# Performance work log

Hardware: AMD Instinct MI355X
Metric: run time of the kernel (lower is better)

The kernel has to match this reference:

```python
import jax, jax.numpy as jnp
import numpy as np

K = 64                      # sort-pool k
B_GRAPHS, N_PER = 256, 512  # graphs, nodes per graph
DIM_F, E_PER = 128, 8192    # node feature dim, edges per graph
EMB = 32


def setup_inputs() -> dict:
    key = jax.random.key(0)
    ks = jax.random.split(key, 12)
    N = B_GRAPHS * N_PER
    off = (jnp.arange(B_GRAPHS) * N_PER)[:, None]
    x = jax.random.normal(ks[0], (N, DIM_F), jnp.float32)
    edge_src = (jax.random.randint(ks[1], (B_GRAPHS, E_PER), 0, N_PER) + off).reshape(-1)
    edge_dst = (jax.random.randint(ks[2], (B_GRAPHS, E_PER), 0, N_PER) + off).reshape(-1)

    def lin(k, o, i):
        return (jax.random.normal(k, (o, i), jnp.float32) / np.float32(np.sqrt(i)))

    return {
        "x": x,
        "W0": lin(ks[3], EMB, DIM_F), "b0": jnp.zeros((EMB,), jnp.float32),
        "W1": lin(ks[4], EMB, EMB),   "b1": jnp.zeros((EMB,), jnp.float32),
        "W2": lin(ks[5], EMB, EMB),   "b2": jnp.zeros((EMB,), jnp.float32),
        "W3": lin(ks[6], 1, EMB),     "b3": jnp.zeros((1,), jnp.float32),
        "conv1_w": jax.random.normal(ks[7], (16, 1, 97), jnp.float32) / np.float32(np.sqrt(97.0)),
        "conv1_b": jnp.zeros((16,), jnp.float32),
        "conv2_w": jax.random.normal(ks[8], (32, 16, 5), jnp.float32) / np.float32(np.sqrt(80.0)),
        "conv2_b": jnp.zeros((32,), jnp.float32),
        "d1_w": lin(ks[9], 128, 896),  "d1_b": jnp.zeros((128,), jnp.float32),
        "d2_w": lin(ks[10], 10, 128),  "d2_b": jnp.zeros((10,), jnp.float32),
        "edge_src": edge_src, "edge_dst": edge_dst,
        "num_graphs": B_GRAPHS,
    }


def _dgcnn_conv(h_in, W, b, src, dst):
    # h = lin(x); message = (1/deg_src)[dst] * h[src]; scatter-add at dst
    N = h_in.shape[0]
    h = h_in @ W.T + b
    deg = jax.ops.segment_sum(jnp.ones_like(src, dtype=h.dtype), src, num_segments=N)
    norm = 1.0 / deg                       # self-loops guarantee deg >= 1
    msg = h[src] * norm[dst][:, None]      # [E+N, C]
    return jax.ops.segment_sum(msg, dst, num_segments=N)


def _forward(x, W0, b0, W1, b1, W2, b2, W3, b3,
             conv1_w, conv1_b, conv2_w, conv2_b,
             d1_w, d1_b, d2_w, d2_b, src, dst, num_graphs):
    N = x.shape[0]
    self_idx = jnp.arange(N)
    src = jnp.concatenate([src, self_idx])   # add_self_loops
    dst = jnp.concatenate([dst, self_idx])
    hs = []
    h = x
    for (W, b) in ((W0, b0), (W1, b1), (W2, b2), (W3, b3)):
        h = jnp.tanh(_dgcnn_conv(h, W, b, src, dst))
        hs.append(h)
    feat = jnp.concatenate(hs, axis=1)       # [N, 97]
    D = feat.shape[1]
    B = num_graphs
    n = N // B
    g = feat.reshape(B, n, D)
    # global_sort_pool: sort nodes per graph by last channel, descending, take top-k
    order = jnp.argsort(-g[:, :, -1], axis=1)[:, :K]
    topk = jnp.take_along_axis(g, order[:, :, None], axis=1)   # [B, K, D]
    # Conv1d(1,16,kernel=D,stride=D) over [B,1,K*D] == per-node linear on D
    c1 = jax.nn.relu(jnp.einsum('bkd,od->bok', topk, conv1_w[:, 0, :])
                     + conv1_b[None, :, None])                  # [B,16,K]
    p = c1.reshape(B, 16, K // 2, 2).max(axis=-1)               # MaxPool1d(2,2)
    c2 = jax.lax.conv_general_dilated(p, conv2_w, (1,), 'VALID',
                                      dimension_numbers=('NCH', 'OIH', 'NCH'))
    c2 = jax.nn.relu(c2 + conv2_b[None, :, None])               # [B,32,28]
    flat = c2.reshape(B, -1)                                    # [B,896]
    hid = jax.nn.relu(flat @ d1_w.T + d1_b)                     # dropout = identity (eval)
    return hid @ d2_w.T + d2_b                                  # [B,10]


def reference(x, W0, b0, W1, b1, W2, b2, W3, b3,
              conv1_w, conv1_b, conv2_w, conv2_b,
              d1_w, d1_b, d2_w, d2_b, edge_src, edge_dst, num_graphs):
    return _forward(x, W0, b0, W1, b1, W2, b2, W3, b3,
                    conv1_w, conv1_b, conv2_w, conv2_b,
                    d1_w, d1_b, d2_w, d2_b, edge_src, edge_dst, num_graphs)
```

## Files before the change

kernel.cpp:

```cpp
#include <hip/hip_runtime.h>

#define NG   256
#define NP   512
#define EPG  8192
#define FDIM 128
#define STA  33
#define STB  36

#define OFF_BUFA  0
#define OFF_BUFB  67584
#define OFF_CSR   141312
#define OFF_OFFS  157696
#define OFF_WT    158728
#define OFF_DCNT  158760
#define OFF_NRM   160808
#define SMEM_SZ   162856

#define OFF_KEYA OFF_CSR
#define OFF_IDXA (OFF_CSR + 2048)
#define OFF_KEYB (OFF_CSR + 4096)
#define OFF_IDXB (OFF_CSR + 6144)
#define FO_FEAT 0
#define FO_C1   6208
#define FO_P    7232
#define FO_C2   7744
#define FO_HID  8640

__global__ __launch_bounds__(1024, 4) void dgcnn_fused(
    const float* __restrict__ x,
    const float* __restrict__ W0, const float* __restrict__ b0,
    const float* __restrict__ W1, const float* __restrict__ b1,
    const float* __restrict__ W2, const float* __restrict__ b2,
    const float* __restrict__ W3, const float* __restrict__ b3,
    const float* __restrict__ c1w, const float* __restrict__ c1b,
    const float* __restrict__ c2w, const float* __restrict__ c2b,
    const float* __restrict__ d1w, const float* __restrict__ d1b,
    const float* __restrict__ d2w, const float* __restrict__ d2b,
    const int* __restrict__ esrc, const int* __restrict__ edst,
    float* __restrict__ hs1, float* __restrict__ hs2,
    float* __restrict__ out)
{
  extern __shared__ char smem[];
  float*          stageF = (float*)(smem + OFF_BUFA);
  float*          bufA  = (float*)(smem + OFF_BUFA);
  float*          bufB  = (float*)(smem + OFF_BUFB);
  unsigned short* csr   = (unsigned short*)(smem + OFF_CSR);
  unsigned short* offs  = (unsigned short*)(smem + OFF_OFFS);
  unsigned int*   wt    = (unsigned int*)(smem + OFF_WT);
  unsigned int*   dcnt  = (unsigned int*)(smem + OFF_DCNT);
  float*          nrm   = (float*)(smem + OFF_NRM);
  float*          lin3S = (float*)(smem + OFF_DCNT);
  float*          keyA  = (float*)(smem + OFF_KEYA);
  unsigned int*   idxA  = (unsigned int*)(smem + OFF_IDXA);
  float*          keyB  = (float*)(smem + OFF_KEYB);
  unsigned int*   idxB  = (unsigned int*)(smem + OFF_IDXB);

  const int g    = blockIdx.x;
  const int tid  = threadIdx.x;
  const int lane = tid & 63;
  const int wv   = __builtin_amdgcn_readfirstlane(tid >> 6);
  const int half = __builtin_amdgcn_readfirstlane(tid >> 9);
  const int v    = tid & 511;
  const int nb   = g * NP;
  const size_t gb = (size_t)g * (NP * 32);

  const int ldRow0 = tid >> 3;
  const int ldGrp  = tid & 7;
  const int ldSwz  = (ldGrp ^ (ldRow0 & 7)) * 16;
  const float* xp0 = x + (size_t)nb * FDIM + ldGrp * 4 + (size_t)(ldRow0      ) * FDIM;
  const float* xp1 = x + (size_t)nb * FDIM + ldGrp * 4 + (size_t)(ldRow0 + 128) * FDIM;
  const float* xp2 = x + (size_t)nb * FDIM + ldGrp * 4 + (size_t)(ldRow0 + 256) * FDIM;
  const float* xp3 = x + (size_t)nb * FDIM + ldGrp * 4 + (size_t)(ldRow0 + 384) * FDIM;
  char* sp0 = smem + OFF_BUFA + (ldRow0      ) * 128 + ldSwz;
  char* sp1 = smem + OFF_BUFA + (ldRow0 + 128) * 128 + ldSwz;
  char* sp2 = smem + OFF_BUFA + (ldRow0 + 256) * 128 + ldSwz;
  char* sp3 = smem + OFF_BUFA + (ldRow0 + 384) * 128 + ldSwz;
#define LOADC(kc, r0, r1, r2, r3)                         \
  { r0 = *(const float4*)(xp0 + (kc) * 32);               \
    r1 = *(const float4*)(xp1 + (kc) * 32);               \
    r2 = *(const float4*)(xp2 + (kc) * 32);               \
    r3 = *(const float4*)(xp3 + (kc) * 32); }
#define STOREC(r0, r1, r2, r3)                            \
  { *(float4*)sp0 = r0; *(float4*)sp1 = r1;               \
    *(float4*)sp2 = r2; *(float4*)sp3 = r3; }

  float4 xA0, xA1, xA2, xA3, xB0, xB1, xB2, xB3;
  LOADC(0, xA0, xA1, xA2, xA3);

  if (tid < 512) dcnt[tid] = 0u;
  __syncthreads();

  int es[8], ed[8];
  {
    const int eb = g * EPG;
    const int4* s4 = (const int4*)(esrc + eb);
    const int4* d4 = (const int4*)(edst + eb);
    const int4 sa = s4[tid], sb = s4[tid + 1024];
    const int4 da = d4[tid], db = d4[tid + 1024];
    es[0]=sa.x-nb; es[1]=sa.y-nb; es[2]=sa.z-nb; es[3]=sa.w-nb;
    es[4]=sb.x-nb; es[5]=sb.y-nb; es[6]=sb.z-nb; es[7]=sb.w-nb;
    ed[0]=da.x-nb; ed[1]=da.y-nb; ed[2]=da.z-nb; ed[3]=da.w-nb;
    ed[4]=db.x-nb; ed[5]=db.y-nb; ed[6]=db.z-nb; ed[7]=db.w-nb;
#pragma unroll
    for (int i = 0; i < 8; i++) {
      atomicAdd(&dcnt[es[i]], 1u);
      atomicAdd(&dcnt[ed[i]], 65536u);
    }
  }
  __syncthreads();

  unsigned c_scan = 0;
  if (tid < 512) {
    const unsigned cw = dcnt[tid];
    nrm[tid] = 1.0f / (float)((cw & 0xFFFFu) + 1u);
    dcnt[tid] = 0u;
    c_scan = cw >> 16;
    for (int d = 1; d < 64; d <<= 1) {
      const unsigned t = __shfl_up(c_scan, (unsigned)d, 64);
      if (lane >= d) c_scan += t;
    }
    if (lane == 63) wt[wv] = c_scan;
  }
  __syncthreads();
  if (tid < 512) {
    unsigned base = 0;
    for (int w = 0; w < wv; w++) base += wt[w];
    offs[tid + 1] = (unsigned short)(base + c_scan);
    if (tid == 0) offs[0] = 0;
  }
  __syncthreads();

#pragma unroll
  for (int i = 0; i < 8; i++) {
    const unsigned pos = (unsigned)offs[ed[i]] + atomicAdd(&dcnt[ed[i]], 1u);
    csr[pos] = (unsigned short)es[i];
  }

  float acc0[16];
#pragma unroll
  for (int c = 0; c < 16; c++) acc0[c] = b0[half * 16 + c];
  const char* rowp = smem + OFF_BUFA + v * 128;
  const int vswz = v & 7;
  auto compute_chunk = [&](int kc) {
#pragma unroll
    for (int jg = 0; jg < 8; jg++) {
      const float4 t = *(const float4*)(rowp + ((jg ^ vswz) * 16));
#pragma unroll
      for (int c = 0; c < 16; c++) {
        const float* wr = W0 + (size_t)(half * 16 + c) * FDIM + kc * 32 + jg * 4;
        acc0[c] = fmaf(t.x, wr[0], acc0[c]);
        acc0[c] = fmaf(t.y, wr[1], acc0[c]);
        acc0[c] = fmaf(t.z, wr[2], acc0[c]);
        acc0[c] = fmaf(t.w, wr[3], acc0[c]);
      }
    }
  };
  STOREC(xA0, xA1, xA2, xA3);
  LOADC(1, xB0, xB1, xB2, xB3);
  __syncthreads();
  compute_chunk(0);
  __syncthreads();
  STOREC(xB0, xB1, xB2, xB3);
  LOADC(2, xA0, xA1, xA2, xA3);
  __syncthreads();
  compute_chunk(1);
  __syncthreads();
  STOREC(xA0, xA1, xA2, xA3);
  LOADC(3, xB0, xB1, xB2, xB3);
  __syncthreads();
  compute_chunk(2);
  __syncthreads();
  STOREC(xB0, xB1, xB2, xB3);
  __syncthreads();
  compute_chunk(3);
  {
    float4* br = (float4*)(bufB + v * STB + half * 16);
#pragma unroll
    for (int j = 0; j < 4; j++)
      br[j] = make_float4(acc0[j*4+0], acc0[j*4+1], acc0[j*4+2], acc0[j*4+3]);
  }
  __syncthreads();

  float h[16];
  auto do_agg = [&]() {
    float4 A0, A1, A2, A3;
    const float4* sr = (const float4*)(bufB + v * STB + half * 16);
    A0 = sr[0]; A1 = sr[1]; A2 = sr[2]; A3 = sr[3];
    const int e0 = offs[v], e1 = offs[v + 1];
    int e = e0;
    for (; e + 1 < e1; e += 2) {
      const int s0 = csr[e], s1 = csr[e + 1];
      const float4* rb0 = (const float4*)(bufB + s0 * STB + half * 16);
      const float4* rb1 = (const float4*)(bufB + s1 * STB + half * 16);
      const float4 p0 = rb0[0], p1 = rb0[1], p2 = rb0[2], p3 = rb0[3];
      const float4 q0 = rb1[0], q1 = rb1[1], q2 = rb1[2], q3 = rb1[3];
      A0.x += p0.x + q0.x; A0.y += p0.y + q0.y; A0.z += p0.z + q0.z; A0.w += p0.w + q0.w;
      A1.x += p1.x + q1.x; A1.y += p1.y + q1.y; A1.z += p1.z + q1.z; A1.w += p1.w + q1.w;
      A2.x += p2.x + q2.x; A2.y += p2.y + q2.y; A2.z += p2.z + q2.z; A2.w += p2.w + q2.w;
      A3.x += p3.x + q3.x; A3.y += p3.y + q3.y; A3.z += p3.z + q3.z; A3.w += p3.w + q3.w;
    }
    if (e < e1) {
      const int s = csr[e];
      const float4* rb = (const float4*)(bufB + s * STB + half * 16);
      const float4 r0 = rb[0], r1 = rb[1], r2 = rb[2], r3 = rb[3];
      A0.x += r0.x; A0.y += r0.y; A0.z += r0.z; A0.w += r0.w;
      A1.x += r1.x; A1.y += r1.y; A1.z += r1.z; A1.w += r1.w;
      A2.x += r2.x; A2.y += r2.y; A2.z += r2.z; A2.w += r2.w;
      A3.x += r3.x; A3.y += r3.y; A3.z += r3.z; A3.w += r3.w;
    }
    const float nv = nrm[v];
    h[0]=tanhf(A0.x*nv); h[1]=tanhf(A0.y*nv); h[2]=tanhf(A0.z*nv); h[3]=tanhf(A0.w*nv);
    h[4]=tanhf(A1.x*nv); h[5]=tanhf(A1.y*nv); h[6]=tanhf(A1.z*nv); h[7]=tanhf(A1.w*nv);
    h[8]=tanhf(A2.x*nv); h[9]=tanhf(A2.y*nv); h[10]=tanhf(A2.z*nv); h[11]=tanhf(A2.w*nv);
    h[12]=tanhf(A3.x*nv); h[13]=tanhf(A3.y*nv); h[14]=tanhf(A3.z*nv); h[15]=tanhf(A3.w*nv);
  };

  auto put_hA = [&]() {
    float* aw = bufA + v * STA + half * 16;
#pragma unroll
    for (int j = 0; j < 16; j++) aw[j] = h[j];
  };

  auto spill = [&](float* dst) {
#pragma unroll
    for (int c = 0; c < 16; c++)
      dst[gb + (size_t)(half * 16 + c) * 512 + v] = h[c];
  };

  auto do_lin = [&](const float* __restrict__ W, const float* __restrict__ b) {
    float hf[16];
    const float* ar = bufA + v * STA + (half ^ 1) * 16;
#pragma unroll
    for (int j = 0; j < 16; j++) hf[j] = ar[j];
    float acc[16];
#pragma unroll
    for (int c = 0; c < 16; c++) {
      const int C = half * 16 + c;
      const float* wr = W + C * 32;
      float a = b[C];
#pragma unroll
      for (int j = 0; j < 16; j++) a = fmaf(h[j],  wr[half * 16 + j], a);
#pragma unroll
      for (int j = 0; j < 16; j++) a = fmaf(hf[j], wr[(half ^ 1) * 16 + j], a);
      acc[c] = a;
    }
    float4* br = (float4*)(bufB + v * STB + half * 16);
#pragma unroll
    for (int j = 0; j < 4; j++)
      br[j] = make_float4(acc[j*4+0], acc[j*4+1], acc[j*4+2], acc[j*4+3]);
  };

  do_agg();
  put_hA(); spill(hs1);
  __syncthreads();
  do_lin(W1, b1);
  __syncthreads();
  do_agg();
  put_hA(); spill(hs2);
  __syncthreads();
  do_lin(W2, b2);
  __syncthreads();
  do_agg();
  put_hA();
  __syncthreads();

  if (tid < 512) {
    const float* ar = bufA + tid * STA;
    double a = (double)b3[0];
#pragma unroll
    for (int j = 0; j < 32; j++) a = fma((double)ar[j], (double)W3[j], a);
    lin3S[tid] = (float)a;
  }
  __syncthreads();
  float h4 = 0.f;
  if (tid < 512) {
    double a = (double)lin3S[tid];
    const int e0 = offs[tid], e1 = offs[tid + 1];
    for (int e = e0; e < e1; e++) a += (double)lin3S[csr[e]];
    a *= (double)nrm[tid];
    h4 = tanhf((float)a);
  }
  __syncthreads();

  if (tid < 512) {
    float    sk = h4;
    unsigned si = (unsigned)tid;
#pragma unroll
    for (int kk = 2; kk <= 64; kk <<= 1) {
#pragma unroll
      for (int j = kk >> 1; j > 0; j >>= 1) {
        const float    pk = __shfl_xor(sk, j, 64);
        const unsigned pi = __shfl_xor(si, j, 64);
        const bool amFirst = (sk > pk) || (sk == pk && si < pi);
        const bool lower   = (lane & j) == 0;
        const bool dir     = (lane & kk) == 0;
        const bool keepMine = (lower == dir) ? amFirst : !amFirst;
        if (!keepMine) { sk = pk; si = pi; }
      }
    }
    keyA[tid] = sk;
    idxA[tid] = si;
  }
  __syncthreads();

  auto merge_round = [&](const float* kin, const unsigned* iin,
                         float* kout, unsigned* iout, int L, int R, int O) {
    float    ak = kin[L * 64 + lane];
    unsigned ai = iin[L * 64 + lane];
    float    bk = kin[R * 64 + 63 - lane];
    unsigned bi = iin[R * 64 + 63 - lane];
    float mk; unsigned mi;
    if ((ak > bk) || (ak == bk && ai < bi)) { mk = ak; mi = ai; }
    else                                    { mk = bk; mi = bi; }
#pragma unroll
    for (int j = 32; j > 0; j >>= 1) {
      const float    pk = __shfl_xor(mk, j, 64);
      const unsigned pi = __shfl_xor(mi, j, 64);
      const bool amF   = (mk > pk) || (mk == pk && mi < pi);
      const bool lower = (lane & j) == 0;
      if (lower != amF) { mk = pk; mi = pi; }
    }
    kout[O * 64 + lane] = mk;
    iout[O * 64 + lane] = mi;
  };
  if (wv < 4) merge_round(keyA, idxA, keyB, idxB, 2 * wv, 2 * wv + 1, wv);
  __syncthreads();
  if (wv < 2) merge_round(keyB, idxB, keyA, idxA, 2 * wv, 2 * wv + 1, wv);
  __syncthreads();
  if (wv == 0) merge_round(keyA, idxA, keyB, idxB, 0, 1, 0);
  __syncthreads();

  {
    float* featS = stageF + FO_FEAT;
    const int k = tid >> 4, t = tid & 15;
    const int node = (int)idxB[k];
    float vals[7];
#pragma unroll
    for (int m = 0; m < 7; m++) {
      const int d = t + 16 * m;
      float val = 0.f;
      if (d < 32)       val = hs1[gb + (size_t)d * 512 + node];
      else if (d < 64)  val = hs2[gb + (size_t)(d - 32) * 512 + node];
      else if (d < 96)  val = bufA[node * STA + (d - 64)];
      else              val = keyB[k];
      vals[m] = val;
    }
    __syncthreads();
#pragma unroll
    for (int m = 0; m < 7; m++) {
      const int d = t + 16 * m;
      if (d < 97) featS[d * 64 + k] = vals[m];
    }
  }
  __syncthreads();

  {
    const float* featS = stageF + FO_FEAT;
    float* c1s = stageF + FO_C1;
    const int ch = wv;
    float a = c1b[ch];
    const float* wr = c1w + ch * 97;
    for (int d = 0; d < 97; d++)
      a = fmaf(featS[d * 64 + lane], wr[d], a);
    c1s[ch * 64 + lane] = fmaxf(a, 0.f);
  }
  __syncthreads();

  if (tid < 512) {
    const float* c1s = stageF + FO_C1;
    float* ps  = stageF + FO_P;
    const int o = tid >> 5, jj = tid & 31;
    ps[o * 32 + jj] = fmaxf(c1s[o * 64 + 2 * jj], c1s[o * 64 + 2 * jj + 1]);
  }
  __syncthreads();

  {
    const float* ps  = stageF + FO_P;
    float* c2s = stageF + FO_C2;
    const int o = wv;
    if (lane < 28) {
      float a0 = 0.f, a1 = 0.f;
      for (int i = 0; i < 16; i++) {
#pragma unroll
        for (int r = 0; r < 5; r++) {
          const float pv = ps[i * 32 + lane + r];
          a0 = fmaf(pv, c2w[((o     ) * 16 + i) * 5 + r], a0);
          a1 = fmaf(pv, c2w[((o + 16) * 16 + i) * 5 + r], a1);
        }
      }
      c2s[(o     ) * 28 + lane] = fmaxf(a0 + c2b[o     ], 0.f);
      c2s[(o + 16) * 28 + lane] = fmaxf(a1 + c2b[o + 16], 0.f);
    }
  }
  __syncthreads();

  {
    const float* c2s  = stageF + FO_C2;
    float* hids = stageF + FO_HID;
    float fl[14];
#pragma unroll
    for (int j = 0; j < 14; j++) fl[j] = c2s[lane + j * 64];
    for (int hh = 0; hh < 8; hh++) {
      const int hI = wv * 8 + hh;
      const float* wr = d1w + (size_t)hI * 896;
      float a = 0.f;
#pragma unroll
      for (int j = 0; j < 14; j++) a = fmaf(fl[j], wr[lane + j * 64], a);
#pragma unroll
      for (int m = 32; m > 0; m >>= 1) a += __shfl_xor(a, m, 64);
      if (lane == 0) hids[hI] = fmaxf(a + d1b[hI], 0.f);
    }
  }
  __syncthreads();

  if (tid < 10) {
    const float* hids = stageF + FO_HID;
    const float* wr = d2w + tid * 128;
    float a = d2b[tid];
#pragma unroll 8
    for (int hh = 0; hh < 128; hh++) a = fmaf(hids[hh], wr[hh], a);
    out[g * 10 + tid] = a;
  }
}

extern "C" void kernel_launch(void* const* d_in, const int* in_sizes, int n_in,
                              void* d_out, int out_size, void* d_ws, size_t ws_size,
                              hipStream_t stream) {
  const float* x   = (const float*)d_in[0];
  const float* W0  = (const float*)d_in[1];
  const float* b0  = (const float*)d_in[2];
  const float* W1  = (const float*)d_in[3];
  const float* b1  = (const float*)d_in[4];
  const float* W2  = (const float*)d_in[5];
  const float* b2  = (const float*)d_in[6];
  const float* W3  = (const float*)d_in[7];
  const float* b3  = (const float*)d_in[8];
  const float* c1w = (const float*)d_in[9];
  const float* c1b = (const float*)d_in[10];
  const float* c2w = (const float*)d_in[11];
  const float* c2b = (const float*)d_in[12];
  const float* d1w = (const float*)d_in[13];
  const float* d1b = (const float*)d_in[14];
  const float* d2w = (const float*)d_in[15];
  const float* d2b = (const float*)d_in[16];
  const int* esrc  = (const int*)d_in[17];
  const int* edst  = (const int*)d_in[18];

  float* hs1 = (float*)d_ws;
  float* hs2 = hs1 + (size_t)NG * NP * 32;
  float* outp = (float*)d_out;

  hipFuncSetAttribute(reinterpret_cast<const void*>(dgcnn_fused),
                      hipFuncAttributeMaxDynamicSharedMemorySize, SMEM_SZ);
  dgcnn_fused<<<NG, 1024, SMEM_SZ, stream>>>(x, W0, b0, W1, b1, W2, b2, W3, b3,
                                             c1w, c1b, c2w, c2b, d1w, d1b, d2w, d2b,
                                             esrc, edst, hs1, hs2, outp);
}
```

Measured before the change: 287.0 us.

## Sort nodes by in-degree to balance aggregation work across wavefronts

Builds a per-graph counting sort of nodes by in-degree (histogram, scan, scatter into a permutation) and assigns each thread a permuted node, so lanes in a wavefront walk edge lists of similar length and diverge less in the gather loops. The two halves use mirrored wave order so each half-pair gets a mixed workload. The aggregation loops are also unrolled to four edges with tree adds. The global spills now read back in natural order from shared memory after a barrier. The cost is extra barriers, atomics and permutation bookkeeping, plus more scattered shared-memory access per thread.

```diff
diff --git a/kernel.cpp b/kernel.cpp
--- a/kernel.cpp
+++ b/kernel.cpp
@@ -16,6 +16,8 @@
 #define OFF_NRM   160808
 #define SMEM_SZ   162856
 
+#define OFF_HIST OFF_CSR
+#define OFF_RPRM (OFF_CSR + 256)
 #define OFF_KEYA OFF_CSR
 #define OFF_IDXA (OFF_CSR + 2048)
 #define OFF_KEYB (OFF_CSR + 4096)
@@ -25,6 +27,8 @@
 #define FO_P    7232
 #define FO_C2   7744
 #define FO_HID  8640
+
+#define F4ADD(A,B) { A.x += B.x; A.y += B.y; A.z += B.z; A.w += B.w; }
 
 __global__ __launch_bounds__(1024, 4) void dgcnn_fused(
     const float* __restrict__ x,
@@ -50,6 +54,8 @@
   unsigned int*   dcnt  = (unsigned int*)(smem + OFF_DCNT);
   float*          nrm   = (float*)(smem + OFF_NRM);
   float*          lin3S = (float*)(smem + OFF_DCNT);
+  unsigned int*   hist  = (unsigned int*)(smem + OFF_HIST);
+  unsigned short* rprm  = (unsigned short*)(smem + OFF_RPRM);
   float*          keyA  = (float*)(smem + OFF_KEYA);
   unsigned int*   idxA  = (unsigned int*)(smem + OFF_IDXA);
   float*          keyB  = (float*)(smem + OFF_KEYB);
@@ -60,6 +66,7 @@
   const int lane = tid & 63;
   const int wv   = __builtin_amdgcn_readfirstlane(tid >> 6);
   const int half = __builtin_amdgcn_readfirstlane(tid >> 9);
+  const int hoff = half * 16;
   const int v    = tid & 511;
   const int nb   = g * NP;
   const size_t gb = (size_t)g * (NP * 32);
@@ -88,6 +95,7 @@
   LOADC(0, xA0, xA1, xA2, xA3);
 
   if (tid < 512) dcnt[tid] = 0u;
+  if (tid < 64)  hist[tid] = 0u;
   __syncthreads();
 
   int es[8], ed[8];
@@ -109,12 +117,13 @@
   }
   __syncthreads();
 
-  unsigned c_scan = 0;
+  unsigned c_scan = 0, myindeg = 0;
   if (tid < 512) {
     const unsigned cw = dcnt[tid];
     nrm[tid] = 1.0f / (float)((cw & 0xFFFFu) + 1u);
     dcnt[tid] = 0u;
-    c_scan = cw >> 16;
+    myindeg = cw >> 16;
+    c_scan = myindeg;
     for (int d = 1; d < 64; d <<= 1) {
       const unsigned t = __shfl_up(c_scan, (unsigned)d, 64);
       if (lane >= d) c_scan += t;
@@ -128,6 +137,28 @@
     offs[tid + 1] = (unsigned short)(base + c_scan);
     if (tid == 0) offs[0] = 0;
   }
+
+  const unsigned mybin = (myindeg > 63u) ? 63u : myindeg;
+  __syncthreads();
+  if (tid < 512) atomicAdd(&hist[mybin], 1u);
+  __syncthreads();
+  if (tid < 64) {
+    const unsigned c = hist[tid];
+    unsigned sc = c;
+    for (int d = 1; d < 64; d <<= 1) {
+      const unsigned t = __shfl_up(sc, (unsigned)d, 64);
+      if (lane >= d) sc += t;
+    }
+    hist[tid] = sc - c;
+  }
+  __syncthreads();
+  if (tid < 512) {
+    const unsigned rk = atomicAdd(&hist[mybin], 1u);
+    rprm[rk] = (unsigned short)tid;
+  }
+  __syncthreads();
+  const int rblk = half ? (15 - wv) : wv;
+  const int p    = (int)rprm[rblk * 64 + lane];
   __syncthreads();
 
 #pragma unroll
@@ -138,7 +169,7 @@
 
   float acc0[16];
 #pragma unroll
-  for (int c = 0; c < 16; c++) acc0[c] = b0[half * 16 + c];
+  for (int c = 0; c < 16; c++) acc0[c] = b0[hoff + c];
   const char* rowp = smem + OFF_BUFA + v * 128;
   const int vswz = v & 7;
   auto compute_chunk = [&](int kc) {
@@ -147,7 +178,7 @@
       const float4 t = *(const float4*)(rowp + ((jg ^ vswz) * 16));
 #pragma unroll
       for (int c = 0; c < 16; c++) {
-        const float* wr = W0 + (size_t)(half * 16 + c) * FDIM + kc * 32 + jg * 4;
+        const float* wr = W0 + (size_t)(hoff + c) * FDIM + kc * 32 + jg * 4;
         acc0[c] = fmaf(t.x, wr[0], acc0[c]);
         acc0[c] = fmaf(t.y, wr[1], acc0[c]);
         acc0[c] = fmaf(t.z, wr[2], acc0[c]);
@@ -174,7 +205,7 @@
   __syncthreads();
   compute_chunk(3);
   {
-    float4* br = (float4*)(bufB + v * STB + half * 16);
+    float4* br = (float4*)(bufB + v * STB + hoff);
 #pragma unroll
     for (int j = 0; j < 4; j++)
       br[j] = make_float4(acc0[j*4+0], acc0[j*4+1], acc0[j*4+2], acc0[j*4+3]);
@@ -183,32 +214,32 @@
 
   float h[16];
   auto do_agg = [&]() {
-    float4 A0, A1, A2, A3;
-    const float4* sr = (const float4*)(bufB + v * STB + half * 16);
-    A0 = sr[0]; A1 = sr[1]; A2 = sr[2]; A3 = sr[3];
-    const int e0 = offs[v], e1 = offs[v + 1];
+    const int e0 = offs[p], e1 = offs[p + 1];
+    const float4* sr = (const float4*)(bufB + p * STB + hoff);
+    float4 A0 = sr[0], A1 = sr[1], A2 = sr[2], A3 = sr[3];
     int e = e0;
-    for (; e + 1 < e1; e += 2) {
-      const int s0 = csr[e], s1 = csr[e + 1];
-      const float4* rb0 = (const float4*)(bufB + s0 * STB + half * 16);
-      const float4* rb1 = (const float4*)(bufB + s1 * STB + half * 16);
-      const float4 p0 = rb0[0], p1 = rb0[1], p2 = rb0[2], p3 = rb0[3];
-      const float4 q0 = rb1[0], q1 = rb1[1], q2 = rb1[2], q3 = rb1[3];
-      A0.x += p0.x + q0.x; A0.y += p0.y + q0.y; A0.z += p0.z + q0.z; A0.w += p0.w + q0.w;
-      A1.x += p1.x + q1.x; A1.y += p1.y + q1.y; A1.z += p1.z + q1.z; A1.w += p1.w + q1.w;
-      A2.x += p2.x + q2.x; A2.y += p2.y + q2.y; A2.z += p2.z + q2.z; A2.w += p2.w + q2.w;
-      A3.x += p3.x + q3.x; A3.y += p3.y + q3.y; A3.z += p3.z + q3.z; A3.w += p3.w + q3.w;
-    }
-    if (e < e1) {
+    for (; e + 3 < e1; e += 4) {
+      const int s0 = csr[e], s1 = csr[e + 1], s2 = csr[e + 2], s3 = csr[e + 3];
+      const float4* r0 = (const float4*)(bufB + s0 * STB + hoff);
+      const float4* r1 = (const float4*)(bufB + s1 * STB + hoff);
+      const float4* r2 = (const float4*)(bufB + s2 * STB + hoff);
+      const float4* r3 = (const float4*)(bufB + s3 * STB + hoff);
+      float4 a0 = r0[0], a1 = r0[1], a2 = r0[2], a3 = r0[3];
+      float4 b0v = r1[0], b1v = r1[1], b2v = r1[2], b3v = r1[3];
+      float4 c0 = r2[0], c1 = r2[1], c2 = r2[2], c3 = r2[3];
+      float4 d0 = r3[0], d1 = r3[1], d2 = r3[2], d3 = r3[3];
+      F4ADD(a0, b0v) F4ADD(a1, b1v) F4ADD(a2, b2v) F4ADD(a3, b3v)
+      F4ADD(c0, d0)  F4ADD(c1, d1)  F4ADD(c2, d2)  F4ADD(c3, d3)
+      F4ADD(a0, c0)  F4ADD(a1, c1)  F4ADD(a2, c2)  F4ADD(a3, c3)
+      F4ADD(A0, a0)  F4ADD(A1, a1)  F4ADD(A2, a2)  F4ADD(A3, a3)
+    }
+    for (; e < e1; e++) {
       const int s = csr[e];
-      const float4* rb = (const float4*)(bufB + s * STB + half * 16);
-      const float4 r0 = rb[0], r1 = rb[1], r2 = rb[2], r3 = rb[3];
-      A0.x += r0.x; A0.y += r0.y; A0.z += r0.z; A0.w += r0.w;
-      A1.x += r1.x; A1.y += r1.y; A1.z += r1.z; A1.w += r1.w;
-      A2.x += r2.x; A2.y += r2.y; A2.z += r2.z; A2.w += r2.w;
-      A3.x += r3.x; A3.y += r3.y; A3.z += r3.z; A3.w += r3.w;
-    }
-    const float nv = nrm[v];
+      const float4* rb = (const float4*)(bufB + s * STB + hoff);
+      float4 a0 = rb[0], a1 = rb[1], a2 = rb[2], a3 = rb[3];
+      F4ADD(A0, a0) F4ADD(A1, a1) F4ADD(A2, a2) F4ADD(A3, a3)
+    }
+    const float nv = nrm[p];
     h[0]=tanhf(A0.x*nv); h[1]=tanhf(A0.y*nv); h[2]=tanhf(A0.z*nv); h[3]=tanhf(A0.w*nv);
     h[4]=tanhf(A1.x*nv); h[5]=tanhf(A1.y*nv); h[6]=tanhf(A1.z*nv); h[7]=tanhf(A1.w*nv);
     h[8]=tanhf(A2.x*nv); h[9]=tanhf(A2.y*nv); h[10]=tanhf(A2.z*nv); h[11]=tanhf(A2.w*nv);
@@ -216,53 +247,56 @@
   };
 
   auto put_hA = [&]() {
-    float* aw = bufA + v * STA + half * 16;
+    float* aw = bufA + p * STA + hoff;
 #pragma unroll
     for (int j = 0; j < 16; j++) aw[j] = h[j];
   };
 
-  auto spill = [&](float* dst) {
+  auto spill_nat = [&](float* dst) {
+    const float* ar = bufA + v * STA + hoff;
 #pragma unroll
     for (int c = 0; c < 16; c++)
-      dst[gb + (size_t)(half * 16 + c) * 512 + v] = h[c];
+      dst[gb + (size_t)(hoff + c) * 512 + v] = ar[c];
   };
 
   auto do_lin = [&](const float* __restrict__ W, const float* __restrict__ b) {
     float hf[16];
-    const float* ar = bufA + v * STA + (half ^ 1) * 16;
+    const float* ar = bufA + p * STA + (hoff ^ 16);
 #pragma unroll
     for (int j = 0; j < 16; j++) hf[j] = ar[j];
     float acc[16];
 #pragma unroll
     for (int c = 0; c < 16; c++) {
-      const int C = half * 16 + c;
+      const int C = hoff + c;
       const float* wr = W + C * 32;
       float a = b[C];
 #pragma unroll
-      for (int j = 0; j < 16; j++) a = fmaf(h[j],  wr[half * 16 + j], a);
-#pragma unroll
-      for (int j = 0; j < 16; j++) a = fmaf(hf[j], wr[(half ^ 1) * 16 + j], a);
+      for (int j = 0; j < 16; j++) a = fmaf(h[j],  wr[hoff + j], a);
+#pragma unroll
+      for (int j = 0; j < 16; j++) a = fmaf(hf[j], wr[(hoff ^ 16) + j], a);
       acc[c] = a;
     }
-    float4* br = (float4*)(bufB + v * STB + half * 16);
+    float4* br = (float4*)(bufB + p * STB + hoff);
 #pragma unroll
     for (int j = 0; j < 4; j++)
       br[j] = make_float4(acc[j*4+0], acc[j*4+1], acc[j*4+2], acc[j*4+3]);
   };
 
   do_agg();
-  put_hA(); spill(hs1);
-  __syncthreads();
+  put_hA();
+  __syncthreads();
+  spill_nat(hs1);
   do_lin(W1, b1);
-  __syncthreads();
-  do_agg();
-  put_hA(); spill(hs2);
-  __syncthreads();
-  do_lin(W2, b2);
   __syncthreads();
   do_agg();
   put_hA();
   __syncthreads();
+  spill_nat(hs2);
+  do_lin(W2, b2);
+  __syncthreads();
+  do_agg();
+  put_hA();
+  __syncthreads();
 
   if (tid < 512) {
     const float* ar = bufA + tid * STA;
@@ -274,17 +308,22 @@
   __syncthreads();
   float h4 = 0.f;
   if (tid < 512) {
-    double a = (double)lin3S[tid];
-    const int e0 = offs[tid], e1 = offs[tid + 1];
-    for (int e = e0; e < e1; e++) a += (double)lin3S[csr[e]];
-    a *= (double)nrm[tid];
+    double a = (double)lin3S[p];
+    const int e0 = offs[p], e1 = offs[p + 1];
+    int e = e0;
+    for (; e + 3 < e1; e += 4) {
+      const int s0 = csr[e], s1 = csr[e+1], s2 = csr[e+2], s3 = csr[e+3];
+      a += ((double)lin3S[s0] + (double)lin3S[s1]) + ((double)lin3S[s2] + (double)lin3S[s3]);
+    }
+    for (; e < e1; e++) a += (double)lin3S[csr[e]];
+    a *= (double)nrm[p];
     h4 = tanhf((float)a);
   }
   __syncthreads();
 
   if (tid < 512) {
     float    sk = h4;
-    unsigned si = (unsigned)tid;
+    unsigned si = (unsigned)p;
 #pragma unroll
     for (int kk = 2; kk <= 64; kk <<= 1) {
 #pragma unroll
```

Result: slower. 306.5 us (+6.8%).
